# Kernel tuning notes

Hardware: AMD Instinct MI355X
Metric: run time of the kernel (lower is better)

Reference implementation:

```python
import jax, jax.numpy as jnp
import numpy as np

D_MODEL, D_STATE, D_CONV, EXPAND = 1024, 16, 4, 2
D_INNER = EXPAND * D_MODEL            # 2048
DT_RANK = (D_MODEL + 15) // 16        # 64 (mamba 'auto')
B, L = 2, 2048
EPS = 1e-5


def setup_inputs() -> dict:
    key = jax.random.key(0)
    ks = jax.random.split(key, 12)
    s = lambda k, shape, sc=0.02: jax.random.normal(k, shape, dtype=jnp.float32) * sc
    return {
        "x": jax.random.normal(ks[0], (B, L, D_MODEL), dtype=jnp.float32),
        "ln_w": jnp.ones((D_MODEL,), jnp.float32),
        "ln_b": jnp.zeros((D_MODEL,), jnp.float32),
        "W_in": s(ks[1], (2 * D_INNER, D_MODEL)),
        "conv_w": s(ks[2], (D_INNER, D_CONV), 0.2),
        "conv_b": jnp.zeros((D_INNER,), jnp.float32),
        "W_xproj": s(ks[3], (DT_RANK + 2 * D_STATE, D_INNER)),
        "W_dt": s(ks[4], (D_INNER, DT_RANK), 0.1),
        "b_dt": jax.random.uniform(ks[5], (D_INNER,), jnp.float32, -4.0, -2.0),  # softplus(b)~dt_min
        "A_log": jnp.log(jnp.broadcast_to(jnp.arange(1, D_STATE + 1, dtype=jnp.float32), (D_INNER, D_STATE))),
        "D": jnp.ones((D_INNER,), jnp.float32),
        "W_out": s(ks[6], (D_MODEL, D_INNER)),
    }


def _mamba_forward(x, ln_w, ln_b, W_in, conv_w, conv_b, W_xproj, W_dt, b_dt, A_log, D, W_out):
    # Pre-norm LayerNorm
    mu = jnp.mean(x, axis=-1, keepdims=True)
    var = jnp.mean(jnp.square(x - mu), axis=-1, keepdims=True)
    xn = (x - mu) * jax.lax.rsqrt(var + EPS) * ln_w + ln_b

    # in_proj -> [B, L, 2*d_inner]; split into x-branch and gate z
    xz = jnp.einsum("bld,ed->ble", xn, W_in)
    u, z = jnp.split(xz, 2, axis=-1)

    # causal depthwise conv1d over L, kernel width D_CONV
    u_pad = jnp.pad(u, ((0, 0), (D_CONV - 1, 0), (0, 0)))
    uc = conv_b[None, None, :]
    for k in range(D_CONV):
        uc = uc + u_pad[:, k:k + L, :] * conv_w[:, k]
    u = jax.nn.silu(uc)  # [B, L, d_inner]

    # input-dependent dt, B, C
    dbl = jnp.einsum("bld,ed->ble", u, W_xproj)
    dt_r = dbl[..., :DT_RANK]
    Bm = dbl[..., DT_RANK:DT_RANK + D_STATE]          # [B, L, n]
    Cm = dbl[..., DT_RANK + D_STATE:]                 # [B, L, n]
    dt = jax.nn.softplus(jnp.einsum("blr,dr->bld", dt_r, W_dt) + b_dt)  # [B, L, d]

    A = -jnp.exp(A_log)  # [d, n]

    # selective scan over L; carry h: [B, d, n]
    def step(h, inp):
        dt_t, B_t, C_t, u_t = inp  # [B,d], [B,n], [B,n], [B,d]
        dA = jnp.exp(dt_t[:, :, None] * A[None])                 # [B, d, n]
        h = dA * h + (dt_t * u_t)[:, :, None] * B_t[:, None, :]  # [B, d, n]
        y_t = jnp.einsum("bdn,bn->bd", h, C_t)
        return h, y_t

    xs = (jnp.moveaxis(dt, 1, 0), jnp.moveaxis(Bm, 1, 0),
          jnp.moveaxis(Cm, 1, 0), jnp.moveaxis(u, 1, 0))
    h0 = jnp.zeros((x.shape[0], D_INNER, D_STATE), x.dtype)
    _, ys = jax.lax.scan(step, h0, xs)
    y = jnp.moveaxis(ys, 0, 1) + u * D  # [B, L, d_inner]

    y = y * jax.nn.silu(z)
    out = jnp.einsum("bld,ed->ble", y, W_out)
    return x + out


def reference(x, ln_w, ln_b, W_in, conv_w, conv_b, W_xproj, W_dt, b_dt, A_log, D, W_out):
    return _mamba_forward(x, ln_w, ln_b, W_in, conv_w, conv_b, W_xproj, W_dt, b_dt, A_log, D, W_out)
```

## Files before the change

kernel.cpp:

```cpp
#include <hip/hip_runtime.h>
#include <hip/hip_bf16.h>
#include <stdint.h>

typedef __hip_bfloat16 bf16;
typedef __attribute__((ext_vector_type(8))) short short8;
typedef __attribute__((ext_vector_type(4))) float floatx4;

#define D_MODEL 1024
#define D_STATE 16
#define D_INNER 2048
#define DT_RANK 64
#define BB 2
#define LL 2048
#define BL (BB * LL)
#define XZ_LD (2 * D_INNER)
#define DBL_LD (DT_RANK + 2 * D_STATE)
#define NCH 64
#define TCH (LL / NCH)

__device__ __forceinline__ bf16 f2b(float f) { return __float2bfloat16(f); }

__device__ __forceinline__ float fsig(float v)  { return __fdividef(1.f, 1.f + __expf(-v)); }
__device__ __forceinline__ float fsoftp(float v){ return fmaxf(v, 0.f) + __logf(1.f + __expf(-fabsf(v))); }

__device__ __forceinline__ void gload16(const void* g, void* l) {
    __builtin_amdgcn_global_load_lds(
        (const __attribute__((address_space(1))) uint32_t*)(uintptr_t)g,
        (__attribute__((address_space(3))) uint32_t*)(uintptr_t)l,
        16, 0, 0);
}

#define S0 (4096 * 1024)
#define S1 (128 * 2048)
#define S2 (2048 * 64)
#define S3 (1024 * 2048)
#define S4 (BL * DBL_LD)
#define WCVT_TOT (S0 + S1 + S2 + S3 + S4)

__global__ __launch_bounds__(256) void prep_kernel(
    const float* __restrict__ x, const float* __restrict__ w,
    const float* __restrict__ b, bf16* __restrict__ xnb,
    const float* __restrict__ Win, const float* __restrict__ Wx,
    const float* __restrict__ Wdt, const float* __restrict__ Wout,
    bf16* __restrict__ win_bf, bf16* __restrict__ wx_bf,
    bf16* __restrict__ wdt_bf, bf16* __restrict__ wout_bf,
    float* __restrict__ dbl)
{
    __shared__ float s1[256], s2[256];
    const int tid = threadIdx.x;
    if (blockIdx.x < BL) {
        const int row = blockIdx.x;
        const float* xr = x + (size_t)row * D_MODEL;
        float v[4], sum = 0.f, sq = 0.f;
#pragma unroll
        for (int i = 0; i < 4; ++i) {
            v[i] = xr[tid + 256 * i];
            sum += v[i];
            sq  += v[i] * v[i];
        }
        s1[tid] = sum; s2[tid] = sq;
        __syncthreads();
        for (int s = 128; s > 0; s >>= 1) {
            if (tid < s) { s1[tid] += s1[tid + s]; s2[tid] += s2[tid + s]; }
            __syncthreads();
        }
        const float mu  = s1[0] * (1.f / D_MODEL);
        const float var = s2[0] * (1.f / D_MODEL) - mu * mu;
        const float rs  = rsqrtf(var + 1e-5f);
#pragma unroll
        for (int i = 0; i < 4; ++i) {
            const int c = tid + 256 * i;
            xnb[(size_t)row * D_MODEL + c] = f2b((v[i] - mu) * rs * w[c] + b[c]);
        }
    } else {
        int id = (blockIdx.x - BL) * 256 + tid;
        if (id < S0) { win_bf[id] = f2b(Win[id]); return; }
        id -= S0;
        if (id < S1) { wx_bf[id] = (id < 96 * 2048) ? f2b(Wx[id]) : f2b(0.f); return; }
        id -= S1;
        if (id < S2) { wdt_bf[id] = f2b(Wdt[id]); return; }
        id -= S2;
        if (id < S3) { wout_bf[id] = f2b(Wout[id]); return; }
        id -= S3;
        dbl[id] = 0.f;
    }
}

#define GTM 128
#define GTN 128
#define GTK 32

template <int EPI>
__global__ __launch_bounds__(256) void gemm_t(
    const bf16* __restrict__ A, int lda,
    const bf16* __restrict__ B, int ldb,
    float* __restrict__ C, int ldc,
    int N, int K,
    const float* __restrict__ bias,
    bf16* __restrict__ C2)
{
    __shared__ short As[GTM * GTK];
    __shared__ short Bs[GTN * GTK];
    const int tid  = threadIdx.x;
    const int lane = tid & 63;
    const int wave = tid >> 6;
    const int wm = (wave & 1) * 64;
    const int wn = (wave >> 1) * 64;
    const int bm = blockIdx.y * GTM;
    const int bn = blockIdx.x * GTN;
    const int kbase = blockIdx.z * K;

    floatx4 acc[4][4];
#pragma unroll
    for (int i = 0; i < 4; ++i)
#pragma unroll
        for (int j = 0; j < 4; ++j) acc[i][j] = (floatx4){0.f, 0.f, 0.f, 0.f};

    const int srow = wave * 16 + (lane >> 2);
    const int scol = (lane & 3) * 8;
    const int fm = lane & 15;
    const int q  = lane >> 4;

    for (int k0 = 0; k0 < K; k0 += GTK) {
#pragma unroll
        for (int r = 0; r < 2; ++r) {
            const int m = r * 64 + srow;
            gload16(A + (size_t)(bm + m) * lda + kbase + k0 + scol,
                    As + m * GTK + scol);
            gload16(B + (size_t)(bn + m) * ldb + kbase + k0 + scol,
                    Bs + m * GTK + scol);
        }
        __syncthreads();

        short8 af[4], bfr[4];
#pragma unroll
        for (int i = 0; i < 4; ++i)
            af[i] = *(short8*)&As[(wm + i * 16 + fm) * GTK + q * 8];
#pragma unroll
        for (int j = 0; j < 4; ++j)
            bfr[j] = *(short8*)&Bs[(wn + j * 16 + fm) * GTK + q * 8];
#pragma unroll
        for (int i = 0; i < 4; ++i)
#pragma unroll
            for (int j = 0; j < 4; ++j)
                acc[i][j] = __builtin_amdgcn_mfma_f32_16x16x32_bf16(
                    af[i], bfr[j], acc[i][j], 0, 0, 0);
        __syncthreads();
    }

    const int col = lane & 15;
    const int rq  = (lane >> 4) * 4;
#pragma unroll
    for (int i = 0; i < 4; ++i) {
#pragma unroll
        for (int j = 0; j < 4; ++j) {
#pragma unroll
            for (int r = 0; r < 4; ++r) {
                const int gm = bm + wm + i * 16 + rq + r;
                const int gn = bn + wn + j * 16 + col;
                if (gn >= N) continue;
                float v = acc[i][j][r];
                if constexpr (EPI == 3) {
                    atomicAdd(&C[(size_t)gm * ldc + gn], v);
                } else if constexpr (EPI == 4) {
                    if (gn < D_INNER) C[(size_t)gm * ldc + gn] = v;
                    else C2[(size_t)gm * (size_t)D_INNER + (gn - D_INNER)] = f2b(v);
                } else {
                    C2[(size_t)gm * ldc + gn] = f2b(fsoftp(v + bias[gn]));
                }
            }
        }
    }
}

#define OTM 128
#define OTN 64

__global__ __launch_bounds__(256) void gemm_out(
    const bf16* __restrict__ A, int lda,
    const bf16* __restrict__ B, int ldb,
    const float* __restrict__ resid,
    float* __restrict__ C)
{
    __shared__ short As[OTM * GTK];
    __shared__ short Bs[OTN * GTK];
    const int tid  = threadIdx.x;
    const int lane = tid & 63;
    const int wave = tid >> 6;
    const int wm = (wave & 1) * 64;
    const int wn = (wave >> 1) * 32;
    const int bm = blockIdx.y * OTM;
    const int bn = blockIdx.x * OTN;

    floatx4 acc[4][2];
#pragma unroll
    for (int i = 0; i < 4; ++i)
#pragma unroll
        for (int j = 0; j < 2; ++j) acc[i][j] = (floatx4){0.f, 0.f, 0.f, 0.f};

    const int srow = wave * 16 + (lane >> 2);
    const int scol = (lane & 3) * 8;
    const int fm = lane & 15;
    const int q  = lane >> 4;

    for (int k0 = 0; k0 < D_INNER; k0 += GTK) {
        gload16(A + (size_t)(bm + srow) * lda + k0 + scol,
                As + srow * GTK + scol);
        gload16(A + (size_t)(bm + 64 + srow) * lda + k0 + scol,
                As + (64 + srow) * GTK + scol);
        gload16(B + (size_t)(bn + srow) * ldb + k0 + scol,
                Bs + srow * GTK + scol);
        __syncthreads();

        short8 af[4], bfr[2];
#pragma unroll
        for (int i = 0; i < 4; ++i)
            af[i] = *(short8*)&As[(wm + i * 16 + fm) * GTK + q * 8];
#pragma unroll
        for (int j = 0; j < 2; ++j)
            bfr[j] = *(short8*)&Bs[(wn + j * 16 + fm) * GTK + q * 8];
#pragma unroll
        for (int i = 0; i < 4; ++i)
#pragma unroll
            for (int j = 0; j < 2; ++j)
                acc[i][j] = __builtin_amdgcn_mfma_f32_16x16x32_bf16(
                    af[i], bfr[j], acc[i][j], 0, 0, 0);
        __syncthreads();
    }

    const int col = lane & 15;
    const int rq  = (lane >> 4) * 4;
#pragma unroll
    for (int i = 0; i < 4; ++i) {
#pragma unroll
        for (int j = 0; j < 2; ++j) {
#pragma unroll
            for (int r = 0; r < 4; ++r) {
                const int gm = bm + wm + i * 16 + rq + r;
                const int gn = bn + wn + j * 16 + col;
                C[(size_t)gm * D_MODEL + gn] =
                    acc[i][j][r] + resid[(size_t)gm * D_MODEL + gn];
            }
        }
    }
}

__global__ __launch_bounds__(256) void conv_par3(
    const float* __restrict__ uraw, const float* __restrict__ cw,
    const float* __restrict__ cb, bf16* __restrict__ ucb)
{
    const int id = blockIdx.x * 256 + threadIdx.x;
    const int d = id & (D_INNER - 1);
    const int t = (id >> 11) & (LL - 1);
    float acc = cb[d];
#pragma unroll
    for (int k = 0; k < 4; ++k) {
        const int tt = t - 3 + k;
        if (tt >= 0)
            acc += uraw[(size_t)id + (size_t)(k - 3) * D_INNER] * cw[d * 4 + k];
    }
    ucb[id] = f2b(acc * fsig(acc));
}

__global__ __launch_bounds__(256) void cvt_dtr(
    const float* __restrict__ dbl, bf16* __restrict__ dtr_bf)
{
    const int id = blockIdx.x * 256 + threadIdx.x;
    const int m = id >> 6, r = id & 63;
    dtr_bf[id] = f2b(dbl[(size_t)m * DBL_LD + r]);
}

__global__ __launch_bounds__(256) void scan_p1(
    const bf16* __restrict__ uc, const bf16* __restrict__ dtb,
    const float* __restrict__ dbl, const float* __restrict__ A_log,
    float* __restrict__ Psum, float* __restrict__ Hloc)
{
    const int blk = blockIdx.x;
    const int d = (blk & 7) * 256 + threadIdx.x;
    const int c = (blk >> 3) & (NCH - 1);
    const int b = blk >> 9;
    float A[D_STATE], h[D_STATE];
    bool lin = true;
#pragma unroll
    for (int n = 0; n < D_STATE; ++n) {
        A[n] = -__expf(A_log[d * D_STATE + n]);
        lin = lin && (fabsf(A[n] + (float)(n + 1)) < 1e-3f);
        h[n] = 0.f;
    }
    const size_t row0 = (size_t)b * LL + c * TCH;
    const bf16* dtp = dtb + row0 * D_INNER + d;
    const bf16* up  = uc  + row0 * D_INNER + d;
    const float* Bp = dbl + row0 * DBL_LD + DT_RANK;
    float S = 0.f;
    if (lin) {
        for (int t = 0; t < TCH; ++t) {
            const float dtv = (float)dtp[(size_t)t * D_INNER];
            const float uv  = (float)up[(size_t)t * D_INNER];
            const float du  = dtv * uv;
            S += dtv;
            const float e1 = __expf(-dtv);
            float dA = 1.f;
#pragma unroll
            for (int n = 0; n < D_STATE; ++n) {
                dA *= e1;
                h[n] = dA * h[n] + du * Bp[(size_t)t * DBL_LD + n];
            }
        }
    } else {
        for (int t = 0; t < TCH; ++t) {
            const float dtv = (float)dtp[(size_t)t * D_INNER];
            const float uv  = (float)up[(size_t)t * D_INNER];
            const float du  = dtv * uv;
            S += dtv;
#pragma unroll
            for (int n = 0; n < D_STATE; ++n)
                h[n] = __expf(dtv * A[n]) * h[n] + du * Bp[(size_t)t * DBL_LD + n];
        }
    }
    const size_t o = (((size_t)b * NCH + c) * D_INNER + d) * D_STATE;
    if (lin) {
        const float E1 = __expf(-S);
        float P = 1.f;
#pragma unroll
        for (int n = 0; n < D_STATE; ++n) {
            P *= E1;
            Psum[o + n] = P;
            Hloc[o + n] = h[n];
        }
    } else {
#pragma unroll
        for (int n = 0; n < D_STATE; ++n) {
            Psum[o + n] = __expf(S * A[n]);
            Hloc[o + n] = h[n];
        }
    }
}

__global__ __launch_bounds__(256) void scan_p2(
    float* __restrict__ Psum, const float* __restrict__ Hloc)
{
    const int id = blockIdx.x * 256 + threadIdx.x;
    const int dn = id & (D_INNER * D_STATE - 1);
    const int b  = id >> 15;
    float h = 0.f;
    for (int c = 0; c < NCH; ++c) {
        const size_t o = ((size_t)(b * NCH + c) * D_INNER * D_STATE) + dn;
        const float P  = Psum[o];
        const float hl = Hloc[o];
        Psum[o] = h;
        h = P * h + hl;
    }
}

__global__ __launch_bounds__(256) void scan_p3b(
    bf16* __restrict__ ucy, const bf16* __restrict__ dtb,
    const float* __restrict__ dbl, const float* __restrict__ A_log,
    const float* __restrict__ Dw, const float* __restrict__ Hin,
    const bf16* __restrict__ zbf)
{
    const int blk = blockIdx.x;
    const int d = (blk & 7) * 256 + threadIdx.x;
    const int c = (blk >> 3) & (NCH - 1);
    const int b = blk >> 9;
    float A[D_STATE], h[D_STATE];
    const size_t o = (((size_t)b * NCH + c) * D_INNER + d) * D_STATE;
    bool lin = true;
#pragma unroll
    for (int n = 0; n < D_STATE; ++n) {
        A[n] = -__expf(A_log[d * D_STATE + n]);
        lin = lin && (fabsf(A[n] + (float)(n + 1)) < 1e-3f);
        h[n] = Hin[o + n];
    }
    const float Dd = Dw[d];
    const size_t row0 = (size_t)b * LL + c * TCH;
    const bf16* dtp = dtb + row0 * D_INNER + d;
    bf16*       uyp = ucy + row0 * D_INNER + d;
    const float* BCp = dbl + row0 * DBL_LD;
    const bf16* zp   = zbf + row0 * D_INNER + d;
    if (lin) {
        for (int t = 0; t < TCH; ++t) {
            const float dtv = (float)dtp[(size_t)t * D_INNER];
            const float uv  = (float)uyp[(size_t)t * D_INNER];
            const float du  = dtv * uv;
            float acc = uv * Dd;
            const float* Brow = BCp + (size_t)t * DBL_LD + DT_RANK;
            const float* Crow = Brow + D_STATE;
            const float e1 = __expf(-dtv);
            float dA = 1.f;
#pragma unroll
            for (int n = 0; n < D_STATE; ++n) {
                dA *= e1;
                h[n] = dA * h[n] + du * Brow[n];
                acc += h[n] * Crow[n];
            }
            const float zv = (float)zp[(size_t)t * D_INNER];
            uyp[(size_t)t * D_INNER] = f2b(acc * zv * fsig(zv));
        }
    } else {
        for (int t = 0; t < TCH; ++t) {
            const float dtv = (float)dtp[(size_t)t * D_INNER];
            const float uv  = (float)uyp[(size_t)t * D_INNER];
            const float du  = dtv * uv;
            float acc = uv * Dd;
            const float* Brow = BCp + (size_t)t * DBL_LD + DT_RANK;
            const float* Crow = Brow + D_STATE;
#pragma unroll
            for (int n = 0; n < D_STATE; ++n) {
                h[n] = __expf(dtv * A[n]) * h[n] + du * Brow[n];
                acc += h[n] * Crow[n];
            }
            const float zv = (float)zp[(size_t)t * D_INNER];
            uyp[(size_t)t * D_INNER] = f2b(acc * zv * fsig(zv));
        }
    }
}

#define BM 128
#define BN 128
#define BK 8

__global__ __launch_bounds__(256) void ln_kernel(
    const float* __restrict__ x, const float* __restrict__ w,
    const float* __restrict__ b, float* __restrict__ xnf)
{
    __shared__ float s1[256], s2[256];
    const int row = blockIdx.x;
    const int tid = threadIdx.x;
    const float* xr = x + (size_t)row * D_MODEL;
    float v[4], sum = 0.f, sq = 0.f;
#pragma unroll
    for (int i = 0; i < 4; ++i) {
        v[i] = xr[tid + 256 * i];
        sum += v[i];
        sq  += v[i] * v[i];
    }
    s1[tid] = sum; s2[tid] = sq;
    __syncthreads();
    for (int s = 128; s > 0; s >>= 1) {
        if (tid < s) { s1[tid] += s1[tid + s]; s2[tid] += s2[tid + s]; }
        __syncthreads();
    }
    const float mu  = s1[0] * (1.f / D_MODEL);
    const float var = s2[0] * (1.f / D_MODEL) - mu * mu;
    const float rs  = rsqrtf(var + 1e-5f);
#pragma unroll
    for (int i = 0; i < 4; ++i) {
        const int c = tid + 256 * i;
        xnf[(size_t)row * D_MODEL + c] = (v[i] - mu) * rs * w[c] + b[c];
    }
}

__global__ __launch_bounds__(256) void gemm_bt(
    const float* __restrict__ A, int lda,
    const float* __restrict__ Bw,
    float* __restrict__ C, int ldc,
    int M, int N, int K, int epi,
    const float* __restrict__ bias,
    const float* __restrict__ resid)
{
    __shared__ float As[BK][BM + 1];
    __shared__ float Bs[BK][BN + 1];
    const int tx = threadIdx.x, ty = threadIdx.y;
    const int tid = ty * 16 + tx;
    const int bm = blockIdx.y * BM, bn = blockIdx.x * BN;
    float acc[8][8];
#pragma unroll
    for (int i = 0; i < 8; ++i)
#pragma unroll
        for (int j = 0; j < 8; ++j) acc[i][j] = 0.f;
    for (int k0 = 0; k0 < K; k0 += BK) {
#pragma unroll
        for (int i = tid; i < BM * BK; i += 256) {
            const int m = i / BK, kk = i % BK;
            As[kk][m] = A[(size_t)(bm + m) * lda + (k0 + kk)];
        }
#pragma unroll
        for (int i = tid; i < BN * BK; i += 256) {
            const int n = i / BK, kk = i % BK;
            const int gn = bn + n;
            Bs[kk][n] = (gn < N) ? Bw[(size_t)gn * K + (k0 + kk)] : 0.f;
        }
        __syncthreads();
#pragma unroll
        for (int kk = 0; kk < BK; ++kk) {
            float av[8], bv[8];
#pragma unroll
            for (int i = 0; i < 8; ++i) av[i] = As[kk][ty * 8 + i];
#pragma unroll
            for (int j = 0; j < 8; ++j) bv[j] = Bs[kk][tx * 8 + j];
#pragma unroll
            for (int i = 0; i < 8; ++i)
#pragma unroll
                for (int j = 0; j < 8; ++j) acc[i][j] += av[i] * bv[j];
        }
        __syncthreads();
    }
#pragma unroll
    for (int i = 0; i < 8; ++i) {
        const int gm = bm + ty * 8 + i;
#pragma unroll
        for (int j = 0; j < 8; ++j) {
            const int gn = bn + tx * 8 + j;
            if (gn >= N) continue;
            float v = acc[i][j];
            if (epi == 1) {
                v += bias[gn];
                v = fmaxf(v, 0.f) + log1pf(expf(-fabsf(v)));
            } else if (epi == 2) {
                v += resid[(size_t)gm * ldc + gn];
            }
            C[(size_t)gm * ldc + gn] = v;
        }
    }
}

__global__ __launch_bounds__(256) void conv_silu_kernel(
    float* __restrict__ xz, const float* __restrict__ cw,
    const float* __restrict__ cb)
{
    const int idx = blockIdx.x * 256 + threadIdx.x;
    const int b = idx >> 11, d = idx & (D_INNER - 1);
    const float w0 = cw[d * 4 + 0], w1 = cw[d * 4 + 1];
    const float w2 = cw[d * 4 + 2], w3 = cw[d * 4 + 3];
    const float bias = cb[d];
    float* u = xz + (size_t)b * LL * XZ_LD + d;
    float x0 = 0.f, x1 = 0.f, x2 = 0.f;
    for (int t = 0; t < LL; ++t) {
        const float x3 = u[(size_t)t * XZ_LD];
        const float c = bias + x0 * w0 + x1 * w1 + x2 * w2 + x3 * w3;
        u[(size_t)t * XZ_LD] = c / (1.f + expf(-c));
        x0 = x1; x1 = x2; x2 = x3;
    }
}

__global__ __launch_bounds__(256) void scan_kernel(
    float* __restrict__ xz, const float* __restrict__ dtb,
    const float* __restrict__ dbl,
    const float* __restrict__ A_log, const float* __restrict__ Dw)
{
    const int idx = blockIdx.x * 256 + threadIdx.x;
    const int b = idx >> 11, d = idx & (D_INNER - 1);
    float A[D_STATE], h[D_STATE];
#pragma unroll
    for (int n = 0; n < D_STATE; ++n) {
        A[n] = -expf(A_log[d * D_STATE + n]);
        h[n] = 0.f;
    }
    const float Dd = Dw[d];
    const float* dtp  = dtb + (size_t)b * LL * D_INNER + d;
    float*       up   = xz  + (size_t)b * LL * XZ_LD + d;
    const float* dblp = dbl + (size_t)b * LL * DBL_LD;
    for (int t = 0; t < LL; ++t) {
        const float dtv = dtp[(size_t)t * D_INNER];
        const float uv  = up[(size_t)t * XZ_LD];
        const float zv  = up[(size_t)t * XZ_LD + D_INNER];
        const float* Brow = dblp + (size_t)t * DBL_LD + DT_RANK;
        const float* Crow = Brow + D_STATE;
        const float du = dtv * uv;
        float acc = uv * Dd;
#pragma unroll
        for (int n = 0; n < D_STATE; ++n) {
            const float dA = expf(dtv * A[n]);
            h[n] = dA * h[n] + du * Brow[n];
            acc += h[n] * Crow[n];
        }
        const float sz = zv / (1.f + expf(-zv));
        up[(size_t)t * XZ_LD] = acc * sz;
    }
}

extern "C" void kernel_launch(void* const* d_in, const int* in_sizes, int n_in,
                              void* d_out, int out_size, void* d_ws, size_t ws_size,
                              hipStream_t stream)
{
    const float* x       = (const float*)d_in[0];
    const float* ln_w    = (const float*)d_in[1];
    const float* ln_b    = (const float*)d_in[2];
    const float* W_in    = (const float*)d_in[3];
    const float* conv_w  = (const float*)d_in[4];
    const float* conv_b  = (const float*)d_in[5];
    const float* W_xproj = (const float*)d_in[6];
    const float* W_dt    = (const float*)d_in[7];
    const float* b_dt    = (const float*)d_in[8];
    const float* A_log   = (const float*)d_in[9];
    const float* Dw      = (const float*)d_in[10];
    const float* W_out   = (const float*)d_in[11];
    float* out = (float*)d_out;

    float* wsf     = (float*)d_ws;
    bf16*  dtb_bf  = (bf16*)wsf;
    float* uraw    = wsf + 4194304;
    bf16*  zbf     = (bf16*)(wsf + 12582912);
    float* Psum    = wsf + 16777216;
    float* Hloc    = wsf + 20971520;
    float* dbl     = wsf + 25165824;
    bf16*  ucy     = (bf16*)(wsf + 25559040);
    bf16*  xn_bf   = (bf16*)(wsf + 29753344);
    bf16*  win_bf  = (bf16*)(wsf + 31850496);
    bf16*  wx_bf   = (bf16*)(wsf + 33947648);
    bf16*  wdt_bf  = (bf16*)(wsf + 34078720);
    bf16*  wout_bf = (bf16*)(wsf + 34144256);
    bf16*  dtr_bf  = (bf16*)(wsf + 35192832);
    const size_t need_big = (size_t)35323904 * sizeof(float);

    if (ws_size >= need_big) {
        prep_kernel<<<BL + WCVT_TOT / 256, 256, 0, stream>>>(
            x, ln_w, ln_b, xn_bf,
            W_in, W_xproj, W_dt, W_out, win_bf, wx_bf, wdt_bf, wout_bf, dbl);
        gemm_t<4><<<dim3(XZ_LD / GTN, BL / GTM, 1), 256, 0, stream>>>(
            xn_bf, D_MODEL, win_bf, D_MODEL, uraw, D_INNER,
            XZ_LD, D_MODEL, nullptr, zbf);
        conv_par3<<<(size_t)BL * D_INNER / 256, 256, 0, stream>>>(
            uraw, conv_w, conv_b, ucy);
        gemm_t<3><<<dim3(1, BL / GTM, 8), 256, 0, stream>>>(
            ucy, D_INNER, wx_bf, D_INNER, dbl, DBL_LD,
            DBL_LD, D_INNER / 8, nullptr, nullptr);
        cvt_dtr<<<BL * DT_RANK / 256, 256, 0, stream>>>(dbl, dtr_bf);
        gemm_t<5><<<dim3(D_INNER / GTN, BL / GTM, 1), 256, 0, stream>>>(
            dtr_bf, DT_RANK, wdt_bf, DT_RANK, nullptr, D_INNER,
            D_INNER, DT_RANK, b_dt, dtb_bf);
        scan_p1<<<BB * NCH * 8, 256, 0, stream>>>(
            ucy, dtb_bf, dbl, A_log, Psum, Hloc);
        scan_p2<<<BB * D_INNER * D_STATE / 256, 256, 0, stream>>>(Psum, Hloc);
        scan_p3b<<<BB * NCH * 8, 256, 0, stream>>>(
            ucy, dtb_bf, dbl, A_log, Dw, Psum, zbf);
        gemm_out<<<dim3(D_MODEL / OTN, BL / OTM), 256, 0, stream>>>(
            ucy, D_INNER, wout_bf, D_INNER, x, out);
    } else {
        float* fdtb = wsf;
        float* fxn  = fdtb;
        float* fxz  = fdtb + (size_t)BL * D_INNER;
        float* fdbl = fxz + (size_t)BL * XZ_LD;
        ln_kernel<<<BL, 256, 0, stream>>>(x, ln_w, ln_b, fxn);
        dim3 blk(16, 16);
        gemm_bt<<<dim3(XZ_LD / BN, BL / BM), blk, 0, stream>>>(
            fxn, D_MODEL, W_in, fxz, XZ_LD, BL, XZ_LD, D_MODEL, 0, nullptr, nullptr);
        conv_silu_kernel<<<(BB * D_INNER) / 256, 256, 0, stream>>>(fxz, conv_w, conv_b);
        gemm_bt<<<dim3(1, BL / BM), blk, 0, stream>>>(
            fxz, XZ_LD, W_xproj, fdbl, DBL_LD, BL, DBL_LD, D_INNER, 0, nullptr, nullptr);
        gemm_bt<<<dim3(D_INNER / BN, BL / BM), blk, 0, stream>>>(
            fdbl, DBL_LD, W_dt, fdtb, D_INNER, BL, D_INNER, DT_RANK, 1, b_dt, nullptr);
        scan_kernel<<<(BB * D_INNER) / 256, 256, 0, stream>>>(fxz, fdtb, fdbl, A_log, Dw);
        gemm_bt<<<dim3(D_MODEL / BN, BL / BM), blk, 0, stream>>>(
            fxz, XZ_LD, W_out, out, D_MODEL, BL, D_MODEL, D_INNER, 2, nullptr, x);
    }
}
```

Before: 345.4 us.

## Replace in_proj GEMM with 256x256-tile double-buffered MFMA kernel

Adds a dedicated in_proj GEMM kernel that uses 256x256 output tiles with 512 threads, XOR-swizzled LDS and double-buffered global-to-LDS loads interleaved with MFMA issue, and a block-index remap for L2 locality. It replaces the generic templated GEMM for the xn·W_in product, aiming to raise data reuse per tile and hide load latency. The large 128KB LDS footprint and high register use limit occupancy, and the 256 blocks fill the GPU with only about one wave of work.

```diff
diff --git a/kernel.cpp b/kernel.cpp
--- a/kernel.cpp
+++ b/kernel.cpp
@@ -170,6 +170,125 @@
                 }
             }
         }
+    }
+}
+
+#define PNT (D_MODEL / 64)
+
+__global__ __launch_bounds__(512, 2) void gemm256_uz(
+    const bf16* __restrict__ A,
+    const bf16* __restrict__ B,
+    float* __restrict__ U,
+    bf16* __restrict__ Z)
+{
+    __shared__ __attribute__((aligned(16))) short lds[65536];
+    const int t    = threadIdx.x;
+    const int lane = t & 63;
+    const int wid  = t >> 6;
+    const int wm   = wid >> 2;
+    const int wn   = wid & 3;
+    const int fm   = lane & 15;
+    const int q    = lane >> 4;
+
+    const int lin = (int)blockIdx.x;
+    const int nid = (lin & 7) * 32 + (lin >> 3);
+    const int bm  = (nid >> 4) * 256;
+    const int bn  = (nid & 15) * 256;
+
+    const int sg   = (((t & 7) ^ ((t >> 3) & 7)) << 3);
+    const int ldst = t * 8;
+    const short* Agp = (const short*)A + (size_t)(bm + (t >> 3)) * D_MODEL + sg;
+    const short* Bgp = (const short*)B + (size_t)(bn + (t >> 3)) * D_MODEL + sg;
+
+#define STG(g, lb) do { \
+        gload16((g),                           &lds[(lb) + ldst]);        \
+        gload16((g) + (size_t)64 * D_MODEL,    &lds[(lb) + 4096 + ldst]); \
+    } while (0)
+
+    const int ss0 = ((q ^ (fm & 7)) << 3);
+    const int ss1 = (((4 + q) ^ (fm & 7)) << 3);
+    const int aro = fm * 64;
+    const int bro = ((wn & 1) * 64 + fm) * 64;
+
+    floatx4 acc[8][4];
+#pragma unroll
+    for (int i = 0; i < 8; ++i)
+#pragma unroll
+        for (int j = 0; j < 4; ++j) acc[i][j] = (floatx4){0.f, 0.f, 0.f, 0.f};
+
+    STG(Agp, 0);
+    STG(Agp + (size_t)128 * D_MODEL, 8192);
+    STG(Bgp, 32768);
+    STG(Bgp + (size_t)128 * D_MODEL, 32768 + 8192);
+
+    for (int kt = 0; kt < PNT; ++kt) {
+        __syncthreads();
+        const int d  = kt & 1;
+        const short* Ab = &lds[d * 16384 + wm * 8192];
+        const short* Bb = &lds[32768 + d * 16384 + (wn >> 1) * 8192];
+        const int kn = (kt + 1) * 64;
+        const int nb = (d ^ 1) * 16384;
+
+        short8 bfr[4][2];
+#pragma unroll
+        for (int cf = 0; cf < 4; ++cf) {
+            bfr[cf][0] = *(const short8*)(Bb + bro + cf * 1024 + ss0);
+            bfr[cf][1] = *(const short8*)(Bb + bro + cf * 1024 + ss1);
+        }
+
+#pragma unroll
+        for (int qd = 0; qd < 4; ++qd) {
+            short8 af[2][2];
+#pragma unroll
+            for (int i = 0; i < 2; ++i) {
+                af[i][0] = *(const short8*)(Ab + (qd * 2 + i) * 1024 + aro + ss0);
+                af[i][1] = *(const short8*)(Ab + (qd * 2 + i) * 1024 + aro + ss1);
+            }
+            if (qd == 0 && kt < PNT - 1) {
+                STG(Agp + kn,                        nb);
+                STG(Agp + (size_t)128 * D_MODEL + kn, nb + 8192);
+            }
+            if (qd == 1 && kt < PNT - 1) {
+                STG(Bgp + kn,                        32768 + nb);
+                STG(Bgp + (size_t)128 * D_MODEL + kn, 32768 + nb + 8192);
+            }
+            __builtin_amdgcn_s_barrier();
+            __builtin_amdgcn_s_setprio(1);
+#pragma unroll
+            for (int i = 0; i < 2; ++i)
+#pragma unroll
+                for (int cf = 0; cf < 4; ++cf) {
+                    acc[qd * 2 + i][cf] = __builtin_amdgcn_mfma_f32_16x16x32_bf16(
+                        af[i][0], bfr[cf][0], acc[qd * 2 + i][cf], 0, 0, 0);
+                    acc[qd * 2 + i][cf] = __builtin_amdgcn_mfma_f32_16x16x32_bf16(
+                        af[i][1], bfr[cf][1], acc[qd * 2 + i][cf], 0, 0, 0);
+                }
+            __builtin_amdgcn_s_setprio(0);
+            if (qd < 3) __builtin_amdgcn_s_barrier();
+        }
+    }
+#undef STG
+
+    const int gm0 = bm + wm * 128 + q * 4;
+    const int gn0 = bn + wn * 64 + fm;
+    if (bn < D_INNER) {
+#pragma unroll
+        for (int rf = 0; rf < 8; ++rf)
+#pragma unroll
+            for (int cf = 0; cf < 4; ++cf)
+#pragma unroll
+                for (int r = 0; r < 4; ++r)
+                    U[(size_t)(gm0 + rf * 16 + r) * D_INNER + gn0 + cf * 16] =
+                        acc[rf][cf][r];
+    } else {
+#pragma unroll
+        for (int rf = 0; rf < 8; ++rf)
+#pragma unroll
+            for (int cf = 0; cf < 4; ++cf)
+#pragma unroll
+                for (int r = 0; r < 4; ++r)
+                    Z[(size_t)(gm0 + rf * 16 + r) * D_INNER + gn0 + cf * 16 - D_INNER] =
+                        f2b(acc[rf][cf][r]);
     }
 }
 
@@ -607,9 +726,7 @@
         prep_kernel<<<BL + WCVT_TOT / 256, 256, 0, stream>>>(
             x, ln_w, ln_b, xn_bf,
             W_in, W_xproj, W_dt, W_out, win_bf, wx_bf, wdt_bf, wout_bf, dbl);
-        gemm_t<4><<<dim3(XZ_LD / GTN, BL / GTM, 1), 256, 0, stream>>>(
-            xn_bf, D_MODEL, win_bf, D_MODEL, uraw, D_INNER,
-            XZ_LD, D_MODEL, nullptr, zbf);
+        gemm256_uz<<<dim3(256), 512, 0, stream>>>(xn_bf, win_bf, uraw, zbf);
         conv_par3<<<(size_t)BL * D_INNER / 256, 256, 0, stream>>>(
             uraw, conv_w, conv_b, ucy);
         gemm_t<3><<<dim3(1, BL / GTM, 8), 256, 0, stream>>>(
```

After: 322.2 us. 1.07x faster.
